# Kernel tuning notes

Measured on AMD Instinct MI355X. Metric: run time of the kernel, lower is better.

Reference implementation:

```python
import jax, jax.numpy as jnp
import numpy as np

N_MEL = 80
N_TEXT = 256
N_ATT = 80
N_OUT = 256
B, T_MEL, T_TEXT = 32, 2048, 512


def setup_inputs() -> dict:
    key = jax.random.key(0)
    ks = jax.random.split(key, 16)
    inp = {
        "queries": jax.random.normal(ks[0], (B, T_MEL, N_MEL), dtype=jnp.float32),
        "keys": jax.random.normal(ks[1], (B, T_TEXT, N_TEXT), dtype=jnp.float32),
        "values": jax.random.normal(ks[2], (B, T_TEXT, N_TEXT), dtype=jnp.float32),
        "attention_mask": jnp.ones((B, T_TEXT), dtype=bool),
        "prior": jax.random.uniform(ks[3], (B, T_MEL, T_TEXT), dtype=jnp.float32),
        # learned params (stored as [in, out] so x @ W matches torch's x @ W.T)
        "Wq": jax.random.normal(ks[4], (N_MEL, N_ATT), dtype=jnp.float32) * (1.0 / np.sqrt(N_MEL)),
        "bq": jnp.zeros((N_ATT,), dtype=jnp.float32),
        "Wk": jax.random.normal(ks[5], (N_TEXT, N_ATT), dtype=jnp.float32) * (1.0 / np.sqrt(N_TEXT)),
        "bk": jnp.zeros((N_ATT,), dtype=jnp.float32),
        "Wv": jax.random.normal(ks[6], (N_TEXT, N_ATT), dtype=jnp.float32) * (1.0 / np.sqrt(N_TEXT)),
        "bv": jnp.zeros((N_ATT,), dtype=jnp.float32),
        "Wo": jax.random.normal(ks[7], (N_ATT, N_OUT), dtype=jnp.float32) * (1.0 / np.sqrt(N_ATT)),
        "bo": jnp.zeros((N_OUT,), dtype=jnp.float32),
    }
    return inp


def reference(queries, keys, values, attention_mask, prior,
              Wq, bq, Wk, bk, Wv, bv, Wo, bo):
    # attn_scale = sqrt(sqrt(n_att_channels)); applied to both q and k
    scale = jnp.asarray(N_ATT, jnp.float32) ** 0.25
    q = (queries @ Wq + bq) / scale            # [B, T_mel, d]
    k = (keys @ Wk + bk) / scale               # [B, T_text, d]
    v = values @ Wv + bv                       # [B, T_text, d]
    scores = jnp.einsum("bmd,btd->bmt", q, k)  # [B, T_mel, T_text]
    scores = jnp.where(attention_mask[:, None, :], scores, -jnp.inf)
    # prior-weighted double softmax: log_softmax + log(prior), then softmax
    scores = jax.nn.log_softmax(scores, axis=-1) + jnp.log(prior + 1e-8)
    soft_attn = jax.nn.softmax(scores, axis=-1)
    context = jnp.einsum("bmt,btd->bmd", soft_attn, v)  # [B, T_mel, d]
    output_states = context @ Wo + bo                    # [B, T_mel, 256]
    # dropout=0.0, binarize=False -> attention_probs == soft_attn
    return (output_states, soft_attn, soft_attn)
```

## Files before the change

kernel.cpp:

```cpp
#include <hip/hip_runtime.h>
#include <hip/hip_bf16.h>
#include <math.h>

#define BATCH 32
#define TMEL  2048
#define TTEXT 512
#define DD    80
#define DP    96
#define NOUT  256
#define NK    256

typedef short bf16x8 __attribute__((ext_vector_type(8)));
typedef float f32x4  __attribute__((ext_vector_type(4)));
typedef int   i32x4  __attribute__((ext_vector_type(4)));
typedef unsigned short u16x4 __attribute__((ext_vector_type(4)));
typedef unsigned short u16x8 __attribute__((ext_vector_type(8)));

static __device__ __forceinline__ unsigned short f2b(float x) {
  __hip_bfloat16 h = __float2bfloat16(x);
  return __builtin_bit_cast(unsigned short, h);
}
static __device__ __forceinline__ float b2f(unsigned short h) {
  unsigned u = (unsigned)h << 16;
  return __builtin_bit_cast(float, u);
}
static __device__ __forceinline__ bf16x8 ldb(const unsigned short* p) {
  return *reinterpret_cast<const bf16x8*>(p);
}
static __device__ __forceinline__ bf16x8 cvt8(const float* p) {
  f32x4 a = *reinterpret_cast<const f32x4*>(p);
  f32x4 c = *reinterpret_cast<const f32x4*>(p + 4);
  bf16x8 v;
  #pragma unroll
  for (int r = 0; r < 4; ++r) {
    v[r]     = (short)f2b(a[r]);
    v[r + 4] = (short)f2b(c[r]);
  }
  return v;
}
static __device__ __forceinline__ void st_nt(float* p, f32x4 v) {
  __builtin_nontemporal_store(v, reinterpret_cast<f32x4*>(p));
}

static __device__ __forceinline__ void barrier_lgkm() {
  asm volatile("s_waitcnt lgkmcnt(0)" ::: "memory");
  __builtin_amdgcn_s_barrier();
  __builtin_amdgcn_sched_barrier(0);
}

__global__ __launch_bounds__(256) void prep_w_kernel(
    const float* __restrict__ Wq, const float* __restrict__ Wk,
    const float* __restrict__ Wv, const float* __restrict__ Wo,
    unsigned short* __restrict__ Wqt, unsigned short* __restrict__ Wkt,
    unsigned short* __restrict__ Wvt, unsigned short* __restrict__ Wot)
{
  int i = blockIdx.x * 256 + threadIdx.x;
  if (i < DD * DP) {
    int d = i / DP, k = i - d * DP;
    Wqt[i] = (k < DD) ? f2b(Wq[k * DD + d]) : (unsigned short)0;
  }
  if (i < DD * NK) {
    int d = i / NK, k = i - d * NK;
    Wkt[i] = f2b(Wk[(size_t)k * DD + d]);
    Wvt[i] = f2b(Wv[(size_t)k * DD + d]);
  }
  if (i < NOUT * DP) {
    int n = i / DP, k = i - n * DP;
    Wot[i] = (k < DD) ? f2b(Wo[(size_t)k * NOUT + n]) : (unsigned short)0;
  }
}

__global__ __launch_bounds__(64) void proj_q_kernel(
    const float* __restrict__ queries, const unsigned short* __restrict__ Wqt,
    const float* __restrict__ bq, unsigned short* __restrict__ Qp, float inv_scale)
{
  const int lane = threadIdx.x, lhi = lane >> 4, llo = lane & 15;
  const size_t row0 = (size_t)blockIdx.x * 16;
  const float* Xr = queries + (row0 + llo) * DD;

  bf16x8 xf0 = cvt8(Xr + lhi * 8);
  bf16x8 xf1 = cvt8(Xr + 32 + lhi * 8);
  bf16x8 xf2 = {};
  if (lhi < 2) xf2 = cvt8(Xr + 64 + lhi * 8);

  f32x4 acc[5] = {};
  #pragma unroll
  for (int dt = 0; dt < 5; ++dt) {
    const unsigned short* Wr = Wqt + (dt * 16 + llo) * DP + lhi * 8;
    acc[dt] = __builtin_amdgcn_mfma_f32_16x16x32_bf16(ldb(Wr),      xf0, acc[dt], 0, 0, 0);
    acc[dt] = __builtin_amdgcn_mfma_f32_16x16x32_bf16(ldb(Wr + 32), xf1, acc[dt], 0, 0, 0);
    acc[dt] = __builtin_amdgcn_mfma_f32_16x16x32_bf16(ldb(Wr + 64), xf2, acc[dt], 0, 0, 0);
  }
  unsigned short* Qr = Qp + (row0 + llo) * DP;
  #pragma unroll
  for (int dt = 0; dt < 5; ++dt) {
    f32x4 b4 = *reinterpret_cast<const f32x4*>(bq + dt * 16 + lhi * 4);
    u16x4 h4;
    #pragma unroll
    for (int r = 0; r < 4; ++r) h4[r] = f2b((acc[dt][r] + b4[r]) * inv_scale);
    *reinterpret_cast<u16x4*>(Qr + dt * 16 + lhi * 4) = h4;
  }
  if (lhi == 0) {
    u16x8 z8 = {};
    *reinterpret_cast<u16x8*>(Qr + 80) = z8;
    *reinterpret_cast<u16x8*>(Qr + 88) = z8;
  }
}

__global__ __launch_bounds__(64) void proj_kv_kernel(
    const float* __restrict__ keys, const float* __restrict__ values,
    const unsigned short* __restrict__ Wkt, const unsigned short* __restrict__ Wvt,
    const float* __restrict__ bk, const float* __restrict__ bv,
    unsigned short* __restrict__ Kp, unsigned short* __restrict__ Vt, float inv_scale)
{
  const int lane = threadIdx.x, lhi = lane >> 4, llo = lane & 15;
  const size_t row0 = (size_t)blockIdx.x * 16;
  const int b = (int)(row0 >> 9);
  const int t = (int)(row0 & 511) + llo;

  {
    const float* Kr = keys + (row0 + llo) * NK;
    bf16x8 xf[8];
    #pragma unroll
    for (int ks = 0; ks < 8; ++ks) xf[ks] = cvt8(Kr + ks * 32 + lhi * 8);
    f32x4 acc[5] = {};
    #pragma unroll
    for (int dt = 0; dt < 5; ++dt) {
      const unsigned short* Wr = Wkt + (dt * 16 + llo) * NK + lhi * 8;
      #pragma unroll
      for (int ks = 0; ks < 8; ++ks)
        acc[dt] = __builtin_amdgcn_mfma_f32_16x16x32_bf16(ldb(Wr + ks * 32), xf[ks], acc[dt], 0, 0, 0);
    }
    unsigned short* Krow = Kp + (row0 + llo) * DP;
    #pragma unroll
    for (int dt = 0; dt < 5; ++dt) {
      f32x4 b4 = *reinterpret_cast<const f32x4*>(bk + dt * 16 + lhi * 4);
      u16x4 h4;
      #pragma unroll
      for (int r = 0; r < 4; ++r) h4[r] = f2b((acc[dt][r] + b4[r]) * inv_scale);
      *reinterpret_cast<u16x4*>(Krow + dt * 16 + lhi * 4) = h4;
    }
    if (lhi == 0) {
      u16x8 z8 = {};
      *reinterpret_cast<u16x8*>(Krow + 80) = z8;
      *reinterpret_cast<u16x8*>(Krow + 88) = z8;
    }
  }
  {
    const float* Vr = values + (row0 + llo) * NK;
    bf16x8 xf[8];
    #pragma unroll
    for (int ks = 0; ks < 8; ++ks) xf[ks] = cvt8(Vr + ks * 32 + lhi * 8);
    f32x4 acc[5] = {};
    #pragma unroll
    for (int dt = 0; dt < 5; ++dt) {
      const unsigned short* Wr = Wvt + (dt * 16 + llo) * NK + lhi * 8;
      #pragma unroll
      for (int ks = 0; ks < 8; ++ks)
        acc[dt] = __builtin_amdgcn_mfma_f32_16x16x32_bf16(ldb(Wr + ks * 32), xf[ks], acc[dt], 0, 0, 0);
    }
    #pragma unroll
    for (int dt = 0; dt < 5; ++dt) {
      f32x4 b4 = *reinterpret_cast<const f32x4*>(bv + dt * 16 + lhi * 4);
      #pragma unroll
      for (int r = 0; r < 4; ++r) {
        int d = dt * 16 + lhi * 4 + r;
        Vt[((size_t)b * DD + d) * TTEXT + t] = f2b(acc[dt][r] + b4[r]);
      }
    }
  }
}

__global__ __launch_bounds__(512, 4) void attn_main_kernel(
    const float* __restrict__ prior, const int* __restrict__ mask,
    const unsigned short* __restrict__ Qp, const unsigned short* __restrict__ Kp,
    const unsigned short* __restrict__ Vt, const unsigned short* __restrict__ Wot,
    const float* __restrict__ bo,
    float* __restrict__ out0, float* __restrict__ out1, float* __restrict__ out2)
{
  __shared__ __align__(16) unsigned short s_attn[32][520];
  __shared__ __align__(16) unsigned short s_cbf[32][96];
  float (*s_red)[8][32] = reinterpret_cast<float(*)[8][32]>(&s_cbf[0][0]);

  const int tid = threadIdx.x, w = tid >> 6, lane = tid & 63, lhi = lane >> 4, llo = lane & 15;
  const int b = blockIdx.y, m0 = blockIdx.x * 32;
  const int tb = w * 64;

  const int n0 = w * 32;
  bf16x8 wf[2][3];
  #pragma unroll
  for (int nt = 0; nt < 2; ++nt)
    #pragma unroll
    for (int ks = 0; ks < 3; ++ks)
      wf[nt][ks] = ldb(Wot + (size_t)(n0 + nt * 16 + llo) * DP + ks * 32 + lhi * 8);

  f32x4 z[2][4];
  #pragma unroll
  for (int tt = 0; tt < 4; ++tt) {
    const int t0 = tb + tt * 16 + lhi * 4;
    i32x4 mk4 = *reinterpret_cast<const i32x4*>(&mask[(size_t)b * TTEXT + t0]);
    #pragma unroll
    for (int mt = 0; mt < 2; ++mt) {
      f32x4 p4 = *reinterpret_cast<const f32x4*>(
          &prior[((size_t)b * TMEL + m0 + mt * 16 + llo) * TTEXT + t0]);
      #pragma unroll
      for (int r = 0; r < 4; ++r)
        z[mt][tt][r] = mk4[r] ? __logf(p4[r] + 1e-8f) : -INFINITY;
    }
  }

  bf16x8 qa[2][3];
  const unsigned short* Qb = Qp + ((size_t)b * TMEL + m0) * DP;
  #pragma unroll
  for (int mt = 0; mt < 2; ++mt)
    #pragma unroll
    for (int ks = 0; ks < 3; ++ks)
      qa[mt][ks] = ldb(Qb + (mt * 16 + llo) * DP + ks * 32 + lhi * 8);

  const unsigned short* Kb = Kp + (size_t)b * TTEXT * DP;
  #pragma unroll
  for (int tt = 0; tt < 4; ++tt) {
    int t0 = tb + tt * 16;
    #pragma unroll
    for (int ks = 0; ks < 3; ++ks) {
      bf16x8 kf = ldb(Kb + (size_t)(t0 + llo) * DP + ks * 32 + lhi * 8);
      #pragma unroll
      for (int mt = 0; mt < 2; ++mt)
        z[mt][tt] = __builtin_amdgcn_mfma_f32_16x16x32_bf16(kf, qa[mt][ks], z[mt][tt], 0, 0, 0);
    }
  }

  float mw[2] = {-INFINITY, -INFINITY};
  #pragma unroll
  for (int tt = 0; tt < 4; ++tt)
    #pragma unroll
    for (int mt = 0; mt < 2; ++mt)
      #pragma unroll
      for (int r = 0; r < 4; ++r) mw[mt] = fmaxf(mw[mt], z[mt][tt][r]);
  #pragma unroll
  for (int mt = 0; mt < 2; ++mt) {
    mw[mt] = fmaxf(mw[mt], __shfl_xor(mw[mt], 16));
    mw[mt] = fmaxf(mw[mt], __shfl_xor(mw[mt], 32));
  }
  float sw[2] = {0.f, 0.f};
  #pragma unroll
  for (int tt = 0; tt < 4; ++tt)
    #pragma unroll
    for (int mt = 0; mt < 2; ++mt)
      #pragma unroll
      for (int r = 0; r < 4; ++r) {
        float e = __expf(z[mt][tt][r] - mw[mt]);
        z[mt][tt][r] = e;
        sw[mt] += e;
      }
  #pragma unroll
  for (int mt = 0; mt < 2; ++mt) {
    sw[mt] += __shfl_xor(sw[mt], 16);
    sw[mt] += __shfl_xor(sw[mt], 32);
  }
  if (lane < 16) {
    s_red[0][w][llo] = mw[0];  s_red[0][w][16 + llo] = mw[1];
    s_red[1][w][llo] = sw[0];  s_red[1][w][16 + llo] = sw[1];
  }
  barrier_lgkm();

  float fac[2];
  #pragma unroll
  for (int mt = 0; mt < 2; ++mt) {
    const int idx = mt * 16 + llo;
    float M = s_red[0][0][idx];
    #pragma unroll
    for (int v = 1; v < 8; ++v) M = fmaxf(M, s_red[0][v][idx]);
    float L = 0.f;
    #pragma unroll
    for (int v = 0; v < 8; ++v) L += s_red[1][v][idx] * __expf(s_red[0][v][idx] - M);
    fac[mt] = __expf(mw[mt] - M) / L;
  }

  #pragma unroll
  for (int tt = 0; tt < 4; ++tt) {
    const int t0 = tb + tt * 16 + lhi * 4;
    #pragma unroll
    for (int mt = 0; mt < 2; ++mt) {
      u16x4 h4;
      #pragma unroll
      for (int r = 0; r < 4; ++r) h4[r] = f2b(z[mt][tt][r] * fac[mt]);
      *reinterpret_cast<u16x4*>(&s_attn[mt * 16 + llo][t0]) = h4;
    }
  }
  barrier_lgkm();

  s_cbf[tid >> 4][DD + (tid & 15)] = 0;

  if (w < 5) {
    const unsigned short* Vb = Vt + (size_t)b * DD * TTEXT;
    #pragma unroll
    for (int mt = 0; mt < 2; ++mt) {
      f32x4 pv = {};
      #pragma unroll
      for (int ks = 0; ks < 16; ++ks) {
        bf16x8 af = ldb(&s_attn[mt * 16 + llo][ks * 32 + lhi * 8]);
        bf16x8 vf = ldb(Vb + (size_t)(w * 16 + llo) * TTEXT + ks * 32 + lhi * 8);
        pv = __builtin_amdgcn_mfma_f32_16x16x32_bf16(af, vf, pv, 0, 0, 0);
      }
      #pragma unroll
      for (int r = 0; r < 4; ++r)
        s_cbf[mt * 16 + lhi * 4 + r][w * 16 + llo] = f2b(pv[r]);
    }
  } else {
    const size_t obase = ((size_t)b * TMEL + m0) * TTEXT;
    const int sid = (w - 5) * 64 + lane;
    for (int c = sid; c < 4096; c += 192) {
      const int row = c >> 7, col = (c & 127) << 2;
      u16x4 h4 = *reinterpret_cast<const u16x4*>(&s_attn[row][col]);
      f32x4 a4;
      #pragma unroll
      for (int r = 0; r < 4; ++r) a4[r] = b2f(h4[r]);
      const size_t o = obase + (size_t)row * TTEXT + col;
      st_nt(&out1[o], a4);
      st_nt(&out2[o], a4);
    }
  }
  barrier_lgkm();

  bf16x8 ca[2][3];
  #pragma unroll
  for (int mt = 0; mt < 2; ++mt)
    #pragma unroll
    for (int ks = 0; ks < 3; ++ks)
      ca[mt][ks] = ldb(&s_cbf[mt * 16 + llo][ks * 32 + lhi * 8]);

  #pragma unroll
  for (int nt = 0; nt < 2; ++nt) {
    f32x4 oo[2] = {};
    #pragma unroll
    for (int ks = 0; ks < 3; ++ks) {
      #pragma unroll
      for (int mt = 0; mt < 2; ++mt)
        oo[mt] = __builtin_amdgcn_mfma_f32_16x16x32_bf16(wf[nt][ks], ca[mt][ks], oo[mt], 0, 0, 0);
    }
    f32x4 bo4 = *reinterpret_cast<const f32x4*>(&bo[n0 + nt * 16 + lhi * 4]);
    #pragma unroll
    for (int mt = 0; mt < 2; ++mt) {
      f32x4 res;
      #pragma unroll
      for (int r = 0; r < 4; ++r) res[r] = oo[mt][r] + bo4[r];
      const size_t o = ((size_t)b * TMEL + m0 + mt * 16 + llo) * NOUT + n0 + nt * 16 + lhi * 4;
      st_nt(&out0[o], res);
    }
  }
}

extern "C" void kernel_launch(void* const* d_in, const int* in_sizes, int n_in,
                              void* d_out, int out_size, void* d_ws, size_t ws_size,
                              hipStream_t stream)
{
  (void)in_sizes; (void)n_in; (void)out_size; (void)ws_size;
  const float* queries = (const float*)d_in[0];
  const float* keys    = (const float*)d_in[1];
  const float* values  = (const float*)d_in[2];
  const int*   mask    = (const int*)d_in[3];
  const float* prior   = (const float*)d_in[4];
  const float* Wq = (const float*)d_in[5];
  const float* bq = (const float*)d_in[6];
  const float* Wk = (const float*)d_in[7];
  const float* bk = (const float*)d_in[8];
  const float* Wv = (const float*)d_in[9];
  const float* bv = (const float*)d_in[10];
  const float* Wo = (const float*)d_in[11];
  const float* bo = (const float*)d_in[12];

  float* out0 = (float*)d_out;
  float* out1 = out0 + (size_t)BATCH * TMEL * NOUT;
  float* out2 = out1 + (size_t)BATCH * TMEL * TTEXT;

  unsigned short* Qp  = (unsigned short*)d_ws;
  unsigned short* Kp  = Qp  + (size_t)BATCH * TMEL * DP;
  unsigned short* Vt  = Kp  + (size_t)BATCH * TTEXT * DP;
  unsigned short* Wqt = Vt  + (size_t)BATCH * DD * TTEXT;
  unsigned short* Wkt = Wqt + (size_t)DD * DP;
  unsigned short* Wvt = Wkt + (size_t)DD * NK;
  unsigned short* Wot = Wvt + (size_t)DD * NK;

  const float inv_scale = 1.0f / powf((float)DD, 0.25f);

  prep_w_kernel<<<dim3((NOUT * DP + 255) / 256), 256, 0, stream>>>(
      Wq, Wk, Wv, Wo, Wqt, Wkt, Wvt, Wot);
  proj_q_kernel<<<dim3(BATCH * TMEL / 16), 64, 0, stream>>>(queries, Wqt, bq, Qp, inv_scale);
  proj_kv_kernel<<<dim3(BATCH * TTEXT / 16), 64, 0, stream>>>(
      keys, values, Wkt, Wvt, bk, bv, Kp, Vt, inv_scale);
  attn_main_kernel<<<dim3(TMEL / 32, BATCH), 512, 0, stream>>>(
      prior, mask, Qp, Kp, Vt, Wot, bo, out0, out1, out2);
}
```

Baseline: 134.6 us.

## Fuse query projection into attention kernel and stage output through LDS

Removes the separate query-projection kernel and its bf16 Q workspace round-trip by computing the 32x80 Q tile inside the attention kernel with MFMA and storing it in shared memory aliased over the attention buffer. The full 1/sqrt(d) scale is now applied to K only, so Q needs no scaling. The output projection results are also staged through a swizzled LDS buffer so each row is written to global memory in contiguous, coalesced stores. The cost is extra barriers, reuse of the attention LDS region, and some duplicated query-projection work at the start of each block.

```diff
diff --git a/kernel.cpp b/kernel.cpp
--- a/kernel.cpp
+++ b/kernel.cpp
@@ -70,43 +70,6 @@
   }
 }
 
-__global__ __launch_bounds__(64) void proj_q_kernel(
-    const float* __restrict__ queries, const unsigned short* __restrict__ Wqt,
-    const float* __restrict__ bq, unsigned short* __restrict__ Qp, float inv_scale)
-{
-  const int lane = threadIdx.x, lhi = lane >> 4, llo = lane & 15;
-  const size_t row0 = (size_t)blockIdx.x * 16;
-  const float* Xr = queries + (row0 + llo) * DD;
-
-  bf16x8 xf0 = cvt8(Xr + lhi * 8);
-  bf16x8 xf1 = cvt8(Xr + 32 + lhi * 8);
-  bf16x8 xf2 = {};
-  if (lhi < 2) xf2 = cvt8(Xr + 64 + lhi * 8);
-
-  f32x4 acc[5] = {};
-  #pragma unroll
-  for (int dt = 0; dt < 5; ++dt) {
-    const unsigned short* Wr = Wqt + (dt * 16 + llo) * DP + lhi * 8;
-    acc[dt] = __builtin_amdgcn_mfma_f32_16x16x32_bf16(ldb(Wr),      xf0, acc[dt], 0, 0, 0);
-    acc[dt] = __builtin_amdgcn_mfma_f32_16x16x32_bf16(ldb(Wr + 32), xf1, acc[dt], 0, 0, 0);
-    acc[dt] = __builtin_amdgcn_mfma_f32_16x16x32_bf16(ldb(Wr + 64), xf2, acc[dt], 0, 0, 0);
-  }
-  unsigned short* Qr = Qp + (row0 + llo) * DP;
-  #pragma unroll
-  for (int dt = 0; dt < 5; ++dt) {
-    f32x4 b4 = *reinterpret_cast<const f32x4*>(bq + dt * 16 + lhi * 4);
-    u16x4 h4;
-    #pragma unroll
-    for (int r = 0; r < 4; ++r) h4[r] = f2b((acc[dt][r] + b4[r]) * inv_scale);
-    *reinterpret_cast<u16x4*>(Qr + dt * 16 + lhi * 4) = h4;
-  }
-  if (lhi == 0) {
-    u16x8 z8 = {};
-    *reinterpret_cast<u16x8*>(Qr + 80) = z8;
-    *reinterpret_cast<u16x8*>(Qr + 88) = z8;
-  }
-}
-
 __global__ __launch_bounds__(64) void proj_kv_kernel(
     const float* __restrict__ keys, const float* __restrict__ values,
     const unsigned short* __restrict__ Wkt, const unsigned short* __restrict__ Wvt,
@@ -172,8 +135,10 @@
 }
 
 __global__ __launch_bounds__(512, 4) void attn_main_kernel(
+    const float* __restrict__ queries, const unsigned short* __restrict__ Wqt,
+    const float* __restrict__ bq,
     const float* __restrict__ prior, const int* __restrict__ mask,
-    const unsigned short* __restrict__ Qp, const unsigned short* __restrict__ Kp,
+    const unsigned short* __restrict__ Kp,
     const unsigned short* __restrict__ Vt, const unsigned short* __restrict__ Wot,
     const float* __restrict__ bo,
     float* __restrict__ out0, float* __restrict__ out1, float* __restrict__ out2)
@@ -181,6 +146,8 @@
   __shared__ __align__(16) unsigned short s_attn[32][520];
   __shared__ __align__(16) unsigned short s_cbf[32][96];
   float (*s_red)[8][32] = reinterpret_cast<float(*)[8][32]>(&s_cbf[0][0]);
+  unsigned short (*s_q)[104] = reinterpret_cast<unsigned short(*)[104]>(&s_attn[0][0]);
+  float* s_o = reinterpret_cast<float*>(&s_attn[0][0]);
 
   const int tid = threadIdx.x, w = tid >> 6, lane = tid & 63, lhi = lane >> 4, llo = lane & 15;
   const int b = blockIdx.y, m0 = blockIdx.x * 32;
@@ -194,6 +161,26 @@
     for (int ks = 0; ks < 3; ++ks)
       wf[nt][ks] = ldb(Wot + (size_t)(n0 + nt * 16 + llo) * DP + ks * 32 + lhi * 8);
 
+  for (int j = w; j < 10; j += 8) {
+    const int rowgrp = j / 5, dt = j % 5;
+    const float* Xr = queries + ((size_t)b * TMEL + m0 + rowgrp * 16 + llo) * DD;
+    bf16x8 xf0 = cvt8(Xr + lhi * 8);
+    bf16x8 xf1 = cvt8(Xr + 32 + lhi * 8);
+    bf16x8 xf2 = {};
+    if (lhi < 2) xf2 = cvt8(Xr + 64 + lhi * 8);
+    const unsigned short* Wr = Wqt + (dt * 16 + llo) * DP + lhi * 8;
+    f32x4 acc = {};
+    acc = __builtin_amdgcn_mfma_f32_16x16x32_bf16(ldb(Wr),      xf0, acc, 0, 0, 0);
+    acc = __builtin_amdgcn_mfma_f32_16x16x32_bf16(ldb(Wr + 32), xf1, acc, 0, 0, 0);
+    acc = __builtin_amdgcn_mfma_f32_16x16x32_bf16(ldb(Wr + 64), xf2, acc, 0, 0, 0);
+    f32x4 b4 = *reinterpret_cast<const f32x4*>(bq + dt * 16 + lhi * 4);
+    u16x4 h4;
+    #pragma unroll
+    for (int r = 0; r < 4; ++r) h4[r] = f2b(acc[r] + b4[r]);
+    *reinterpret_cast<u16x4*>(&s_q[rowgrp * 16 + llo][dt * 16 + lhi * 4]) = h4;
+  }
+  s_q[tid >> 4][DD + (tid & 15)] = 0;
+
   f32x4 z[2][4];
   #pragma unroll
   for (int tt = 0; tt < 4; ++tt) {
@@ -209,13 +196,14 @@
     }
   }
 
+  barrier_lgkm();
+
   bf16x8 qa[2][3];
-  const unsigned short* Qb = Qp + ((size_t)b * TMEL + m0) * DP;
   #pragma unroll
   for (int mt = 0; mt < 2; ++mt)
     #pragma unroll
     for (int ks = 0; ks < 3; ++ks)
-      qa[mt][ks] = ldb(Qb + (mt * 16 + llo) * DP + ks * 32 + lhi * 8);
+      qa[mt][ks] = ldb(&s_q[mt * 16 + llo][ks * 32 + lhi * 8]);
 
   const unsigned short* Kb = Kp + (size_t)b * TTEXT * DP;
   #pragma unroll
@@ -342,12 +330,24 @@
     f32x4 bo4 = *reinterpret_cast<const f32x4*>(&bo[n0 + nt * 16 + lhi * 4]);
     #pragma unroll
     for (int mt = 0; mt < 2; ++mt) {
+      const int row = mt * 16 + llo;
+      const int chunk = (w * 8 + nt * 4 + lhi) ^ (row & 7);
       f32x4 res;
       #pragma unroll
       for (int r = 0; r < 4; ++r) res[r] = oo[mt][r] + bo4[r];
-      const size_t o = ((size_t)b * TMEL + m0 + mt * 16 + llo) * NOUT + n0 + nt * 16 + lhi * 4;
-      st_nt(&out0[o], res);
-    }
+      *reinterpret_cast<f32x4*>(&s_o[row * NOUT + chunk * 4]) = res;
+    }
+  }
+  barrier_lgkm();
+
+  const size_t obase0 = ((size_t)b * TMEL + m0) * NOUT;
+  #pragma unroll
+  for (int it = 0; it < 4; ++it) {
+    const int c = tid + it * 512;
+    const int row = c >> 6, chunk = c & 63;
+    const int chunk_sw = chunk ^ (row & 7);
+    f32x4 v = *reinterpret_cast<const f32x4*>(&s_o[row * NOUT + chunk_sw * 4]);
+    st_nt(&out0[obase0 + (size_t)row * NOUT + chunk * 4], v);
   }
 }
 
@@ -374,21 +374,19 @@
   float* out1 = out0 + (size_t)BATCH * TMEL * NOUT;
   float* out2 = out1 + (size_t)BATCH * TMEL * TTEXT;
 
-  unsigned short* Qp  = (unsigned short*)d_ws;
-  unsigned short* Kp  = Qp  + (size_t)BATCH * TMEL * DP;
+  unsigned short* Kp  = (unsigned short*)d_ws;
   unsigned short* Vt  = Kp  + (size_t)BATCH * TTEXT * DP;
   unsigned short* Wqt = Vt  + (size_t)BATCH * DD * TTEXT;
   unsigned short* Wkt = Wqt + (size_t)DD * DP;
   unsigned short* Wvt = Wkt + (size_t)DD * NK;
   unsigned short* Wot = Wvt + (size_t)DD * NK;
 
-  const float inv_scale = 1.0f / powf((float)DD, 0.25f);
+  const float inv_scale = 1.0f / sqrtf((float)DD);
 
   prep_w_kernel<<<dim3((NOUT * DP + 255) / 256), 256, 0, stream>>>(
       Wq, Wk, Wv, Wo, Wqt, Wkt, Wvt, Wot);
-  proj_q_kernel<<<dim3(BATCH * TMEL / 16), 64, 0, stream>>>(queries, Wqt, bq, Qp, inv_scale);
   proj_kv_kernel<<<dim3(BATCH * TTEXT / 16), 64, 0, stream>>>(
       keys, values, Wkt, Wvt, bk, bv, Kp, Vt, inv_scale);
   attn_main_kernel<<<dim3(TMEL / 32, BATCH), 512, 0, stream>>>(
-      prior, mask, Qp, Kp, Vt, Wot, bo, out0, out1, out2);
-}
+      queries, Wqt, bq, prior, mask, Kp, Vt, Wot, bo, out0, out1, out2);
+}
```

After: 120.6 us. -10.4%, faster.
